# Optimization experiments

Measured on AMD Instinct MI355X. Metric: run time of the kernel, lower is better.

## Reference

```python
import jax, jax.numpy as jnp
import numpy as np


def setup_inputs() -> dict:
    key = jax.random.key(0)
    k1, k2 = jax.random.split(key)
    input_tensor = jax.random.normal(k1, (32, 128, 64, 64), dtype=jnp.float32)
    weights = jax.random.normal(k2, (256, 128, 3, 3), dtype=jnp.float32) * 0.05
    return {"input_tensor": input_tensor, "weights": weights}


def reference(input_tensor, weights):
    # Valid-padding, stride-1, no-bias direct conv2d (NCHW x OIHW -> NCHW),
    # identical math to the quintuple-loop slice*weight sum in the original.
    return jax.lax.conv_general_dilated(
        input_tensor,
        weights,
        window_strides=(1, 1),
        padding="VALID",
        dimension_numbers=("NCHW", "OIHW", "NCHW"),
    )
```

## Files before the change

kernel.cpp:

```cpp
#include <hip/hip_runtime.h>
#include <hip/hip_bf16.h>

#define N_IMG 32
#define CIN   128
#define INH   64
#define INW   64
#define COUT  256
#define OH    62
#define OW    62

typedef short          bf16x8 __attribute__((ext_vector_type(8)));
typedef unsigned short u16x8  __attribute__((ext_vector_type(8)));
typedef float          f32x4  __attribute__((ext_vector_type(4)));

__device__ __forceinline__ unsigned short f2bf(float x) {
    unsigned int u = __float_as_uint(x);
    u += 0x7fffu + ((u >> 16) & 1u);
    return (unsigned short)(u >> 16);
}

__global__ void wt_transform_kernel(const float* __restrict__ Wsrc,
                                    unsigned short* __restrict__ WT) {
    int idx = blockIdx.x * 256 + threadIdx.x;
    int i   = idx & 7;
    int co  = (idx >> 3) & 255;
    int cgk = idx >> 11;
    int cg  = cgk & 15;
    int khw = cgk >> 4;
    int kh  = khw / 3, kw = khw - 3 * kh;
    int ci  = cg * 8 + i;
    WT[idx] = f2bf(Wsrc[co * (CIN * 9) + ci * 9 + kh * 3 + kw]);
}

__global__ __launch_bounds__(256, 2)
void conv_mfma_kernel(const float* __restrict__ In,
                      const unsigned short* __restrict__ WT,
                      float* __restrict__ Out) {
    __shared__ unsigned short Lin[66 * 32];

    const int oh   = blockIdx.x;
    const int img  = blockIdx.y;
    const int tid  = threadIdx.x;
    const int wave = tid >> 6;
    const int lane = tid & 63;
    const int q    = lane >> 4;
    const int ml   = lane & 15;
    const int co_base = wave * 64;

    f32x4 acc[4][4];
    const f32x4 zero = {0.f, 0.f, 0.f, 0.f};
#pragma unroll
    for (int a = 0; a < 4; ++a)
#pragma unroll
        for (int b = 0; b < 4; ++b) acc[a][b] = zero;

    if (tid < 32) ((unsigned int*)&Lin[64 * 32])[tid] = 0u;

    const int s_iw = tid & 63;
    const int s_cg = tid >> 6;
    const bf16x8* WTv = (const bf16x8*)WT;

    for (int kh = 0; kh < 3; ++kh) {
        const int ih = oh + kh;
        for (int cb = 0; cb < 4; ++cb) {
            const float* p = In + (((img * CIN + cb * 32 + s_cg * 8) * INH + ih) * INW + s_iw);
            u16x8 v;
#pragma unroll
            for (int i = 0; i < 8; ++i) v[i] = f2bf(p[i * (INH * INW)]);
            __syncthreads();
            *(u16x8*)&Lin[s_iw * 32 + ((s_cg ^ (s_iw & 3)) << 3)] = v;
            __syncthreads();

#pragma unroll
            for (int kw = 0; kw < 3; ++kw) {
                const int khw = kh * 3 + kw;
                bf16x8 wf[4], xf[4];
#pragma unroll
                for (int mi = 0; mi < 4; ++mi)
                    wf[mi] = WTv[(khw * 16 + cb * 4 + q) * 256 + co_base + mi * 16 + ml];
#pragma unroll
                for (int ni = 0; ni < 4; ++ni) {
                    const int row = ni * 16 + ml + kw;
                    xf[ni] = *(const bf16x8*)&Lin[row * 32 + ((q ^ (row & 3)) << 3)];
                }
#pragma unroll
                for (int mi = 0; mi < 4; ++mi)
#pragma unroll
                    for (int ni = 0; ni < 4; ++ni)
                        acc[mi][ni] = __builtin_amdgcn_mfma_f32_16x16x32_bf16(
                            wf[mi], xf[ni], acc[mi][ni], 0, 0, 0);
            }
        }
    }

#pragma unroll
    for (int mi = 0; mi < 4; ++mi) {
#pragma unroll
        for (int r = 0; r < 4; ++r) {
            const int co = co_base + mi * 16 + q * 4 + r;
            float* op = Out + ((img * COUT + co) * OH + oh) * OW;
#pragma unroll
            for (int ni = 0; ni < 4; ++ni) {
                const int ow = ni * 16 + ml;
                if (ow < OW) op[ow] = acc[mi][ni][r];
            }
        }
    }
}

__global__ void conv_naive_kernel(const float* __restrict__ In,
                                  const float* __restrict__ Wt,
                                  float* __restrict__ Out) {
    int idx = blockIdx.x * 256 + threadIdx.x;
    const int total = N_IMG * COUT * OH * OW;
    if (idx >= total) return;
    int ow = idx % OW; int t = idx / OW;
    int oh = t % OH;   t /= OH;
    int co = t % COUT; int img = t / COUT;
    float s = 0.f;
    for (int ci = 0; ci < CIN; ++ci)
#pragma unroll
        for (int kh = 0; kh < 3; ++kh)
#pragma unroll
            for (int kw = 0; kw < 3; ++kw)
                s += In[((img * CIN + ci) * INH + oh + kh) * INW + ow + kw] *
                     Wt[co * CIN * 9 + ci * 9 + kh * 3 + kw];
    Out[idx] = s;
}

extern "C" void kernel_launch(void* const* d_in, const int* in_sizes, int n_in,
                              void* d_out, int out_size, void* d_ws, size_t ws_size,
                              hipStream_t stream) {
    const float* In   = (const float*)d_in[0];
    const float* Wsrc = (const float*)d_in[1];
    float* Out        = (float*)d_out;

    const size_t WT_BYTES = (size_t)9 * 16 * 256 * 8 * sizeof(unsigned short);
    if (ws_size >= WT_BYTES) {
        unsigned short* WT = (unsigned short*)d_ws;
        wt_transform_kernel<<<dim3(294912 / 256), dim3(256), 0, stream>>>(Wsrc, WT);
        conv_mfma_kernel<<<dim3(OH, N_IMG), dim3(256), 0, stream>>>(In, WT, Out);
    } else {
        const int total = N_IMG * COUT * OH * OW;
        conv_naive_kernel<<<dim3((total + 255) / 256), dim3(256), 0, stream>>>(In, Wsrc, Out);
    }
}
```

Baseline: 237.8 us.

## Pre-transform input to swizzled NHWC bf16 and use 32x32 MFMA over two rows

Adds a kernel that converts the fp32 NCHW input once into swizzled NHWC bf16 in the workspace. The conv kernel then bulk-loads four full input rows into LDS with global_load_lds, computes two output rows per block, and switches from 16x16x32 to 32x32x16 bf16 MFMA. This targets the repeated fp32 input reloads and conversions across kh, and the inter-block barriers. The cost is an extra transform pass over the input, a large workspace requirement of about 33 MB, and about 66 KB of LDS per block, which may cap occupancy.

```diff
diff --git a/kernel.cpp b/kernel.cpp
--- a/kernel.cpp
+++ b/kernel.cpp
@@ -12,11 +12,19 @@
 typedef short          bf16x8 __attribute__((ext_vector_type(8)));
 typedef unsigned short u16x8  __attribute__((ext_vector_type(8)));
 typedef float          f32x4  __attribute__((ext_vector_type(4)));
+typedef float          f32x16 __attribute__((ext_vector_type(16)));
 
 __device__ __forceinline__ unsigned short f2bf(float x) {
     unsigned int u = __float_as_uint(x);
     u += 0x7fffu + ((u >> 16) & 1u);
     return (unsigned short)(u >> 16);
+}
+
+__device__ __forceinline__ void gl2lds16(const unsigned short* g, unsigned short* l) {
+    __builtin_amdgcn_global_load_lds(
+        (const __attribute__((address_space(1))) unsigned int*)g,
+        (__attribute__((address_space(3))) unsigned int*)l,
+        16, 0, 0);
 }
 
 __global__ void wt_transform_kernel(const float* __restrict__ Wsrc,
@@ -32,12 +40,131 @@
     WT[idx] = f2bf(Wsrc[co * (CIN * 9) + ci * 9 + kh * 3 + kw]);
 }
 
+__global__ void in_transform_kernel(const float* __restrict__ In,
+                                    unsigned short* __restrict__ InT) {
+    const int ih  = blockIdx.x & 63;
+    const int img = blockIdx.x >> 6;
+    const int t   = threadIdx.x;
+    const int iw  = t & 63;
+    const int cg  = t >> 6;
+    const float* ip = In + (((size_t)img * CIN) * INH + ih) * INW + iw;
+    unsigned short* op = InT + (((size_t)(img * INH + ih) * INW) + iw) * CIN;
+#pragma unroll
+    for (int cc = 0; cc < 4; ++cc) {
+        const int cf = cg * 4 + cc;
+        u16x8 v;
+#pragma unroll
+        for (int j = 0; j < 8; ++j)
+            v[j] = f2bf(ip[(size_t)(cf * 8 + j) * (INH * INW)]);
+        *(u16x8*)(op + ((cf ^ (iw & 15)) * 8)) = v;
+    }
+}
+
 __global__ __launch_bounds__(256, 2)
-void conv_mfma_kernel(const float* __restrict__ In,
-                      const unsigned short* __restrict__ WT,
-                      float* __restrict__ Out) {
+void conv_mfma32_kernel(const unsigned short* __restrict__ InT,
+                        const unsigned short* __restrict__ WT,
+                        float* __restrict__ Out) {
+    __shared__ __align__(16) unsigned short Lin[258 * CIN];
+
+    const int oh0  = blockIdx.x * 2;
+    const int img  = blockIdx.y;
+    const int tid  = threadIdx.x;
+    const int wave = tid >> 6;
+    const int lane = tid & 63;
+    const int h    = lane >> 5;
+    const int m32  = lane & 31;
+    const int co_base = wave * 64;
+
+    {
+        const unsigned short* src =
+            InT + ((size_t)(img * INH + (oh0 + wave)) * INW) * CIN;
+        unsigned short* dst = Lin + wave * (INW * CIN);
+#pragma unroll
+        for (int i = 0; i < 16; ++i)
+            gl2lds16(src + i * 512 + lane * 8, dst + i * 512);
+    }
+    __syncthreads();
+
+    f32x16 acc[2][2][2];
+#pragma unroll
+    for (int a = 0; a < 2; ++a)
+#pragma unroll
+        for (int b = 0; b < 2; ++b)
+#pragma unroll
+            for (int c = 0; c < 2; ++c)
+#pragma unroll
+                for (int g = 0; g < 16; ++g) acc[a][b][c][g] = 0.f;
+
+    const bf16x8* WTv = (const bf16x8*)WT;
+
+    for (int cb = 0; cb < 4; ++cb) {
+#pragma unroll
+        for (int kh = 0; kh < 3; ++kh) {
+#pragma unroll
+            for (int kw = 0; kw < 3; ++kw) {
+                const int khw = kh * 3 + kw;
+                bf16x8 wf[2][2];
+#pragma unroll
+                for (int mi = 0; mi < 2; ++mi)
+#pragma unroll
+                    for (int kc = 0; kc < 2; ++kc)
+                        wf[mi][kc] = WTv[(khw * 16 + cb * 4 + kc * 2 + h) * 256 +
+                                         co_base + mi * 32 + m32];
+                bf16x8 xf[2][2][2];
+#pragma unroll
+                for (int oi = 0; oi < 2; ++oi) {
+                    const int r = oi + kh;
+#pragma unroll
+                    for (int ni = 0; ni < 2; ++ni) {
+                        const int iw = ni * 32 + m32 + kw;
+                        const unsigned short* rp = Lin + (r * 64 + iw) * CIN;
+#pragma unroll
+                        for (int kc = 0; kc < 2; ++kc) {
+                            const int cf = cb * 4 + kc * 2 + h;
+                            xf[oi][ni][kc] =
+                                *(const bf16x8*)(rp + ((cf ^ (iw & 15)) * 8));
+                        }
+                    }
+                }
+#pragma unroll
+                for (int oi = 0; oi < 2; ++oi)
+#pragma unroll
+                    for (int mi = 0; mi < 2; ++mi)
+#pragma unroll
+                        for (int ni = 0; ni < 2; ++ni)
+#pragma unroll
+                            for (int kc = 0; kc < 2; ++kc)
+                                acc[oi][mi][ni] = __builtin_amdgcn_mfma_f32_32x32x16_bf16(
+                                    wf[mi][kc], xf[oi][ni][kc], acc[oi][mi][ni], 0, 0, 0);
+            }
+        }
+    }
+
+#pragma unroll
+    for (int oi = 0; oi < 2; ++oi) {
+        const int oh = oh0 + oi;
+#pragma unroll
+        for (int mi = 0; mi < 2; ++mi) {
+#pragma unroll
+            for (int g = 0; g < 16; ++g) {
+                const int rr = (g & 3) + 8 * (g >> 2) + 4 * h;
+                const int co = co_base + mi * 32 + rr;
+                float* op = Out + (((size_t)img * COUT + co) * OH + oh) * OW;
+#pragma unroll
+                for (int ni = 0; ni < 2; ++ni) {
+                    const int ow = ni * 32 + m32;
+                    if (ow < OW) op[ow] = acc[oi][mi][ni][g];
+                }
+            }
+        }
+    }
+}
+
+__global__ __launch_bounds__(256, 2)
+void conv_mfma16_kernel(const float* __restrict__ In,
+                        const unsigned short* __restrict__ WT,
+                        float* __restrict__ Out) {
     __shared__ unsigned short Lin[66 * 32];
-
     const int oh   = blockIdx.x;
     const int img  = blockIdx.y;
     const int tid  = threadIdx.x;
@@ -53,7 +180,6 @@
     for (int a = 0; a < 4; ++a)
 #pragma unroll
         for (int b = 0; b < 4; ++b) acc[a][b] = zero;
-
     if (tid < 32) ((unsigned int*)&Lin[64 * 32])[tid] = 0u;
 
     const int s_iw = tid & 63;
@@ -63,14 +189,13 @@
     for (int kh = 0; kh < 3; ++kh) {
         const int ih = oh + kh;
         for (int cb = 0; cb < 4; ++cb) {
-            const float* p = In + (((img * CIN + cb * 32 + s_cg * 8) * INH + ih) * INW + s_iw);
+            const float* p = In + (((size_t)(img * CIN + cb * 32 + s_cg * 8) * INH + ih) * INW + s_iw);
             u16x8 v;
 #pragma unroll
             for (int i = 0; i < 8; ++i) v[i] = f2bf(p[i * (INH * INW)]);
             __syncthreads();
             *(u16x8*)&Lin[s_iw * 32 + ((s_cg ^ (s_iw & 3)) << 3)] = v;
             __syncthreads();
-
 #pragma unroll
             for (int kw = 0; kw < 3; ++kw) {
                 const int khw = kh * 3 + kw;
@@ -92,20 +217,18 @@
             }
         }
     }
-
-#pragma unroll
-    for (int mi = 0; mi < 4; ++mi) {
+#pragma unroll
+    for (int mi = 0; mi < 4; ++mi)
 #pragma unroll
         for (int r = 0; r < 4; ++r) {
             const int co = co_base + mi * 16 + q * 4 + r;
-            float* op = Out + ((img * COUT + co) * OH + oh) * OW;
+            float* op = Out + (((size_t)img * COUT + co) * OH + oh) * OW;
 #pragma unroll
             for (int ni = 0; ni < 4; ++ni) {
                 const int ow = ni * 16 + ml;
                 if (ow < OW) op[ow] = acc[mi][ni][r];
             }
         }
-    }
 }
 
 __global__ void conv_naive_kernel(const float* __restrict__ In,
@@ -123,7 +246,7 @@
         for (int kh = 0; kh < 3; ++kh)
 #pragma unroll
             for (int kw = 0; kw < 3; ++kw)
-                s += In[((img * CIN + ci) * INH + oh + kh) * INW + ow + kw] *
+                s += In[((size_t)(img * CIN + ci) * INH + oh + kh) * INW + ow + kw] *
                      Wt[co * CIN * 9 + ci * 9 + kh * 3 + kw];
     Out[idx] = s;
 }
@@ -135,11 +258,20 @@
     const float* Wsrc = (const float*)d_in[1];
     float* Out        = (float*)d_out;
 
-    const size_t WT_BYTES = (size_t)9 * 16 * 256 * 8 * sizeof(unsigned short);
-    if (ws_size >= WT_BYTES) {
+    const size_t WT_BYTES  = (size_t)9 * 16 * 256 * 8 * sizeof(unsigned short);
+    const size_t INT_OFF   = 1u << 20;
+    const size_t INT_BYTES = (size_t)N_IMG * INH * INW * CIN * sizeof(unsigned short);
+
+    if (ws_size >= INT_OFF + INT_BYTES) {
+        unsigned short* WT  = (unsigned short*)d_ws;
+        unsigned short* InT = (unsigned short*)((char*)d_ws + INT_OFF);
+        wt_transform_kernel<<<dim3(294912 / 256), dim3(256), 0, stream>>>(Wsrc, WT);
+        in_transform_kernel<<<dim3(N_IMG * INH), dim3(256), 0, stream>>>(In, InT);
+        conv_mfma32_kernel<<<dim3(OH / 2, N_IMG), dim3(256), 0, stream>>>(InT, WT, Out);
+    } else if (ws_size >= WT_BYTES) {
         unsigned short* WT = (unsigned short*)d_ws;
         wt_transform_kernel<<<dim3(294912 / 256), dim3(256), 0, stream>>>(Wsrc, WT);
-        conv_mfma_kernel<<<dim3(OH, N_IMG), dim3(256), 0, stream>>>(In, WT, Out);
+        conv_mfma16_kernel<<<dim3(OH, N_IMG), dim3(256), 0, stream>>>(In, WT, Out);
     } else {
         const int total = N_IMG * COUT * OH * OW;
         conv_naive_kernel<<<dim3((total + 255) / 256), dim3(256), 0, stream>>>(In, Wsrc, Out);
```

Result: slower. 307.7 us (+29.4%).

## Pre-transpose input to NHWC bf16 and use 32x32 MFMA with LDS DMA

Applied to the files above, without the earlier changes.

Adds a separate kernel that converts the NCHW fp32 input into an NHWC bf16 buffer in the workspace. The conv kernel now loads a swizzled input tile straight into LDS with global_load_lds, computes two output rows per block split into two width halves, and uses 32x32x16 bf16 MFMA instead of 16x16x32. Per-(kh,cb) barriers and the in-kernel fp32-to-bf16 conversion are removed, and the occupancy hint rises to 4 blocks per SM. In exchange it needs an extra kernel pass and more workspace, and the fast path is only taken when the workspace is large enough.

```diff
diff --git a/kernel.cpp b/kernel.cpp
--- a/kernel.cpp
+++ b/kernel.cpp
@@ -11,12 +11,19 @@
 
 typedef short          bf16x8 __attribute__((ext_vector_type(8)));
 typedef unsigned short u16x8  __attribute__((ext_vector_type(8)));
-typedef float          f32x4  __attribute__((ext_vector_type(4)));
+typedef float          f32x16 __attribute__((ext_vector_type(16)));
 
 __device__ __forceinline__ unsigned short f2bf(float x) {
     unsigned int u = __float_as_uint(x);
     u += 0x7fffu + ((u >> 16) & 1u);
     return (unsigned short)(u >> 16);
+}
+
+__device__ __forceinline__ void gl2lds16(const unsigned short* g, unsigned short* l) {
+    __builtin_amdgcn_global_load_lds(
+        (const __attribute__((address_space(1))) unsigned int*)g,
+        (__attribute__((address_space(3))) unsigned int*)l,
+        16, 0, 0);
 }
 
 __global__ void wt_transform_kernel(const float* __restrict__ Wsrc,
@@ -32,77 +39,122 @@
     WT[idx] = f2bf(Wsrc[co * (CIN * 9) + ci * 9 + kh * 3 + kw]);
 }
 
-__global__ __launch_bounds__(256, 2)
-void conv_mfma_kernel(const float* __restrict__ In,
-                      const unsigned short* __restrict__ WT,
-                      float* __restrict__ Out) {
-    __shared__ unsigned short Lin[66 * 32];
-
-    const int oh   = blockIdx.x;
-    const int img  = blockIdx.y;
+__global__ void in_transform_kernel(const float* __restrict__ In,
+                                    unsigned short* __restrict__ InT) {
+    const int q   = blockIdx.x;
+    const int ih  = blockIdx.y;
+    const int img = blockIdx.z;
+    const int t   = threadIdx.x;
+    const int c   = t & 15;
+    const int iwl = t >> 4;
+    const int iw  = q * 16 + iwl;
+    const float* ip = In + (((size_t)img * CIN + c * 8) * INH + ih) * INW + iw;
+    u16x8 v;
+#pragma unroll
+    for (int j = 0; j < 8; ++j) v[j] = f2bf(ip[(size_t)j * INH * INW]);
+    unsigned short* op = InT + (((size_t)(img * INH + ih) * INW) + q * 16) * CIN;
+    *(u16x8*)(op + t * 8) = v;
+}
+
+__global__ __launch_bounds__(256, 4)
+void conv_mfma32_kernel(const unsigned short* __restrict__ InT,
+                        const unsigned short* __restrict__ WT,
+                        float* __restrict__ Out) {
+    __shared__ __align__(16) unsigned short Lin[4 * 4864];
+
+    const int half = blockIdx.x;
+    const int oh0  = blockIdx.y * 2;
+    const int img  = blockIdx.z;
     const int tid  = threadIdx.x;
     const int wave = tid >> 6;
     const int lane = tid & 63;
-    const int q    = lane >> 4;
-    const int ml   = lane & 15;
+    const int h    = lane >> 5;
+    const int m32  = lane & 31;
     const int co_base = wave * 64;
-
-    f32x4 acc[4][4];
-    const f32x4 zero = {0.f, 0.f, 0.f, 0.f};
-#pragma unroll
-    for (int a = 0; a < 4; ++a)
-#pragma unroll
-        for (int b = 0; b < 4; ++b) acc[a][b] = zero;
-
-    if (tid < 32) ((unsigned int*)&Lin[64 * 32])[tid] = 0u;
-
-    const int s_iw = tid & 63;
-    const int s_cg = tid >> 6;
+    const int iw0  = half ? 28 : 0;
+
+    {
+        const unsigned short* gbase =
+            InT + (((size_t)img * INH + oh0) * INW) * CIN;
+#pragma unroll
+        for (int i = 0; i < 9; ++i) {
+            const int k0   = i * 256 + (tid & 192);
+            const int r    = k0 / 576;
+            const int off0 = k0 - r * 576;
+            const int off  = off0 + lane;
+            const int liw  = off >> 4;
+            const int c    = off & 15;
+            const int iw   = iw0 + liw;
+            const int cf   = c ^ (iw & 15);
+            gl2lds16(gbase + (size_t)r * (INW * CIN) + iw * CIN + cf * 8,
+                     Lin + r * 4864 + off0 * 8);
+        }
+    }
+    __syncthreads();
+
+    f32x16 acc[2][2];
+#pragma unroll
+    for (int a = 0; a < 2; ++a)
+#pragma unroll
+        for (int b = 0; b < 2; ++b)
+#pragma unroll
+            for (int g = 0; g < 16; ++g) acc[a][b][g] = 0.f;
+
     const bf16x8* WTv = (const bf16x8*)WT;
-
-    for (int kh = 0; kh < 3; ++kh) {
-        const int ih = oh + kh;
-        for (int cb = 0; cb < 4; ++cb) {
-            const float* p = In + (((img * CIN + cb * 32 + s_cg * 8) * INH + ih) * INW + s_iw);
-            u16x8 v;
-#pragma unroll
-            for (int i = 0; i < 8; ++i) v[i] = f2bf(p[i * (INH * INW)]);
-            __syncthreads();
-            *(u16x8*)&Lin[s_iw * 32 + ((s_cg ^ (s_iw & 3)) << 3)] = v;
-            __syncthreads();
-
+    const int liw_b = m32 + (half ? 4 : 0);
+    const int swz_b = m32 & 15;
+
+    for (int cb = 0; cb < 4; ++cb) {
+#pragma unroll
+        for (int kh = 0; kh < 3; ++kh) {
 #pragma unroll
             for (int kw = 0; kw < 3; ++kw) {
                 const int khw = kh * 3 + kw;
-                bf16x8 wf[4], xf[4];
-#pragma unroll
-                for (int mi = 0; mi < 4; ++mi)
-                    wf[mi] = WTv[(khw * 16 + cb * 4 + q) * 256 + co_base + mi * 16 + ml];
-#pragma unroll
-                for (int ni = 0; ni < 4; ++ni) {
-                    const int row = ni * 16 + ml + kw;
-                    xf[ni] = *(const bf16x8*)&Lin[row * 32 + ((q ^ (row & 3)) << 3)];
+                bf16x8 wf[2][2];
+#pragma unroll
+                for (int mi = 0; mi < 2; ++mi)
+#pragma unroll
+                    for (int kc = 0; kc < 2; ++kc)
+                        wf[mi][kc] = WTv[(khw * 16 + cb * 4 + kc * 2 + h) * 256 +
+                                         co_base + mi * 32 + m32];
+                bf16x8 xf[2][2];
+                const int liw = liw_b + kw;
+                const int swz = (m32 + kw) & 15;
+#pragma unroll
+                for (int oi = 0; oi < 2; ++oi) {
+                    const int r = oi + kh;
+#pragma unroll
+                    for (int kc = 0; kc < 2; ++kc) {
+                        const int cf = cb * 4 + kc * 2 + h;
+                        xf[oi][kc] = *(const bf16x8*)&Lin[r * 4864 + liw * 128 +
+                                                          ((cf ^ swz) * 8)];
+                    }
                 }
 #pragma unroll
-                for (int mi = 0; mi < 4; ++mi)
-#pragma unroll
-                    for (int ni = 0; ni < 4; ++ni)
-                        acc[mi][ni] = __builtin_amdgcn_mfma_f32_16x16x32_bf16(
-                            wf[mi], xf[ni], acc[mi][ni], 0, 0, 0);
+                for (int oi = 0; oi < 2; ++oi)
+#pragma unroll
+                    for (int mi = 0; mi < 2; ++mi)
+#pragma unroll
+                        for (int kc = 0; kc < 2; ++kc)
+                            acc[oi][mi] = __builtin_amdgcn_mfma_f32_32x32x16_bf16(
+                                wf[mi][kc], xf[oi][kc], acc[oi][mi], 0, 0, 0);
             }
         }
     }
 
-#pragma unroll
-    for (int mi = 0; mi < 4; ++mi) {
-#pragma unroll
-        for (int r = 0; r < 4; ++r) {
-            const int co = co_base + mi * 16 + q * 4 + r;
-            float* op = Out + ((img * COUT + co) * OH + oh) * OW;
-#pragma unroll
-            for (int ni = 0; ni < 4; ++ni) {
-                const int ow = ni * 16 + ml;
-                if (ow < OW) op[ow] = acc[mi][ni][r];
+    const int ow = half * 32 + m32;
+#pragma unroll
+    for (int oi = 0; oi < 2; ++oi) {
+        const int oh = oh0 + oi;
+#pragma unroll
+        for (int mi = 0; mi < 2; ++mi) {
+#pragma unroll
+            for (int g = 0; g < 16; ++g) {
+                const int rr = (g & 3) + 8 * (g >> 2) + 4 * h;
+                const int co = co_base + mi * 32 + rr;
+                if (ow < OW)
+                    Out[(((size_t)img * COUT + co) * OH + oh) * OW + ow] =
+                        acc[oi][mi][g];
             }
         }
     }
@@ -123,7 +175,7 @@
         for (int kh = 0; kh < 3; ++kh)
 #pragma unroll
             for (int kw = 0; kw < 3; ++kw)
-                s += In[((img * CIN + ci) * INH + oh + kh) * INW + ow + kw] *
+                s += In[((size_t)(img * CIN + ci) * INH + oh + kh) * INW + ow + kw] *
                      Wt[co * CIN * 9 + ci * 9 + kh * 3 + kw];
     Out[idx] = s;
 }
@@ -135,11 +187,15 @@
     const float* Wsrc = (const float*)d_in[1];
     float* Out        = (float*)d_out;
 
-    const size_t WT_BYTES = (size_t)9 * 16 * 256 * 8 * sizeof(unsigned short);
-    if (ws_size >= WT_BYTES) {
-        unsigned short* WT = (unsigned short*)d_ws;
+    const size_t INT_OFF   = 1u << 20;
+    const size_t INT_BYTES = (size_t)N_IMG * INH * INW * CIN * sizeof(unsigned short);
+
+    if (ws_size >= INT_OFF + INT_BYTES) {
+        unsigned short* WT  = (unsigned short*)d_ws;
+        unsigned short* InT = (unsigned short*)((char*)d_ws + INT_OFF);
         wt_transform_kernel<<<dim3(294912 / 256), dim3(256), 0, stream>>>(Wsrc, WT);
-        conv_mfma_kernel<<<dim3(OH, N_IMG), dim3(256), 0, stream>>>(In, WT, Out);
+        in_transform_kernel<<<dim3(4, INH, N_IMG), dim3(256), 0, stream>>>(In, InT);
+        conv_mfma32_kernel<<<dim3(2, OH / 2, N_IMG), dim3(256), 0, stream>>>(InT, WT, Out);
     } else {
         const int total = N_IMG * COUT * OH * OW;
         conv_naive_kernel<<<dim3((total + 255) / 256), dim3(256), 0, stream>>>(In, Wsrc, Out);
```

New measurement: 380.6 us. 1.6x slower.
